# Performance work log

Measured on AMD Instinct MI355X. Metric: run time of the kernel, lower is better.

The kernel has to match this reference:

```python
import jax, jax.numpy as jnp
import numpy as np

N, G = 50000, 2500
PER = N // G                 # 20 nodes per graph
M, Z, NB, WIDTH, K = 128, 4, 8, 128, 3
INV = 3 * M                  # 384 invariant features
COV = 9 * M                  # 1152 = 128*(1+3+5)
GAMMA = 10.0
D_MIN, D_MAX = 0.9, 1.8
D_CENTER, D_HALF = 0.5 * (D_MIN + D_MAX), 0.5 * (D_MAX - D_MIN)
SQ_MZ = float(np.sqrt(M * Z))  # e3nn path normalization (fan_in = mul1*mul2)
P_GRID = 4096                # Fibonacci sphere quadrature for SO3 normalizer

_i = np.arange(P_GRID)
_ph = np.pi * (3.0 - np.sqrt(5.0)) * _i
_z = 1.0 - 2.0 * (_i + 0.5) / P_GRID
_r = np.sqrt(np.maximum(1.0 - _z * _z, 0.0))
FIB = np.stack([_r * np.cos(_ph), _r * np.sin(_ph), _z], 1).astype(np.float32)

def real_sh(v):
    # real spherical harmonics up to l=2, integral normalization, m=-l..l
    x, y, z = v[..., 0], v[..., 1], v[..., 2]
    c0, c1 = 0.28209479177387814, 0.4886025119029199
    ca, c20, c22 = 1.0925484305920792, 0.31539156525252005, 0.5462742152960396
    return jnp.stack([c0 * jnp.ones_like(x), c1 * y, c1 * z, c1 * x,
                      ca * x * y, ca * y * z, c20 * (3 * z * z - 1.0),
                      ca * x * z, c22 * (x * x - y * y)], -1)

Y_GRID = np.asarray(real_sh(jnp.asarray(FIB)))  # [P_GRID, 9]

def split_cov(x):
    lead = x.shape[:-1]
    return (x[..., :M].reshape(*lead, M, 1),
            x[..., M:4 * M].reshape(*lead, M, 3),
            x[..., 4 * M:9 * M].reshape(*lead, M, 5))

def setup_inputs():
    key = jax.random.key(0)
    ks = jax.random.split(key, 16)
    s_inter = jax.random.normal(ks[0], (N, COV), jnp.float32)
    bag = jnp.floor(jax.random.uniform(ks[1], (G, Z)) * 5.0).at[:, 0].add(1.0)
    batch = jnp.repeat(jnp.arange(G, dtype=jnp.int32), PER)
    ptr = jnp.arange(G + 1, dtype=jnp.int32) * PER
    focus = jax.random.randint(ks[2], (G,), 0, PER, jnp.int32)
    element = jnp.zeros((G,), jnp.int32)  # column 0 of bag is always > 0
    distance = D_MIN + (D_MAX - D_MIN) * jax.random.uniform(ks[3], (G,), jnp.float32)
    ori = jax.random.normal(ks[4], (G, 3), jnp.float32)
    orientation = ori / jnp.linalg.norm(ori, axis=-1, keepdims=True)
    W_bag = jax.random.normal(ks[5], (3, M, Z, M), jnp.float32)
    def lin(k, i, o):
        return jax.random.normal(k, (i, o), jnp.float32) / np.sqrt(i).astype(np.float32)
    return dict(
        s_inter=s_inter, bag=bag, batch=batch, ptr=ptr, focus=focus,
        element=element, distance=distance, orientation=orientation,
        W_bag=W_bag,
        d_log_stds=jnp.full((K,), np.log(0.1), jnp.float32),
        W_mix=jax.random.normal(ks[6], (NB, 3 * M * Z), jnp.float32),
        W1f=lin(ks[7], INV, WIDTH), b1f=jnp.zeros(WIDTH), W2f=lin(ks[8], WIDTH, 1), b2f=jnp.zeros(1),
        W1e=lin(ks[9], INV, WIDTH), b1e=jnp.zeros(WIDTH), W2e=lin(ks[10], WIDTH, Z), b2e=jnp.zeros(Z),
        W1d=lin(ks[11], INV + Z, WIDTH), b1d=jnp.zeros(WIDTH), W2d=lin(ks[12], WIDTH, 2 * K), b2d=jnp.zeros(2 * K),
    )

def reference(s_inter, bag, batch, ptr, focus, element, distance, orientation,
              W_bag, d_log_stds, W_mix,
              W1f, b1f, W2f, b2f, W1e, b1e, W2e, b2e, W1d, b1d, W2d, b2d):
    bag_n = bag[batch]                                  # [N, Z]
    xs = split_cov(s_inter)
    covs = [jnp.einsum('nim,nz,izo->nom', xs[l], bag_n, W_bag[l]) / SQ_MZ for l in range(3)]
    s_cov = jnp.concatenate([c.reshape(N, -1) for c in covs], -1)   # [N, 1152]
    s_inv = jnp.concatenate([jnp.sqrt(jnp.sum(c * c, -1) + 1e-12) for c in covs], -1)  # [N, 384]
    # --- focus: per-graph scatter softmax over nodes ---
    fl = (jax.nn.relu(s_inv @ W1f + b1f) @ W2f + b2f)[:, 0]
    mx = jax.ops.segment_max(fl, batch, num_segments=G)
    ex = jnp.exp(fl - mx[batch])
    focus_probs = ex / jax.ops.segment_sum(ex, batch, num_segments=G)[batch]
    gidx = focus + ptr[:-1]
    lp_focus = jnp.log(focus_probs[gidx] + 1e-20)
    # --- element: bag-masked softmax ---
    el = jax.nn.relu(s_inv @ W1e + b1e) @ W2e + b2e
    mask = (bag > 0)[batch]
    all_element_probs = jax.nn.softmax(jnp.where(mask, el, -1e9), -1)
    foc_el = all_element_probs[gidx]
    lp_element = jnp.log(jnp.take_along_axis(foc_el, element[:, None], 1)[:, 0] + 1e-20)
    element_oh = jax.nn.one_hot(element, Z, dtype=s_inter.dtype)
    # --- distance: Gaussian mixture head ---
    d_in = jnp.concatenate([s_inv[gidx], element_oh], -1)
    h = jax.nn.relu(d_in @ W1d + b1d) @ W2d + b2d
    gmm_logits, d_mean_t = h[:, :K], h[:, K:]
    d_mean = jnp.tanh(d_mean_t) * D_HALF + D_CENTER
    stds = jnp.maximum(jnp.exp(d_log_stds), 1e-6)
    logw = jax.nn.log_softmax(gmm_logits, -1)
    comp = -0.5 * ((distance[:, None] - d_mean) / stds) ** 2 - jnp.log(stds) - 0.5 * np.log(2 * np.pi).astype(np.float32)
    lp_dist = jax.nn.logsumexp(logw + comp, -1)
    # --- mix tensor product with bessel-conditioned external weights ---
    kk = jnp.arange(1, NB + 1, dtype=s_inter.dtype)
    bess = np.sqrt(2.0 / D_MAX).astype(np.float32) * jnp.sin(kk * np.pi * distance[:, None] / D_MAX) / distance[:, None]
    tpw = ((bess @ W_mix) / np.sqrt(NB).astype(np.float32)).reshape(G, 3, M, Z)
    foc = split_cov(s_cov[gidx])
    cond = [jnp.einsum('gim,gz,giz->gm', foc[l], element_oh, tpw[:, l]) / SQ_MZ for l in range(3)]
    cond_cov = jnp.concatenate(cond, -1)                # [G, 9]
    # --- SO(3) distribution: p(x) ~ exp(gamma * <a, Y(x)>), normalized on sphere grid ---
    ori = orientation / jnp.linalg.norm(orientation, axis=-1, keepdims=True)
    f_x = jnp.sum(cond_cov * real_sh(ori), -1)
    f_grid = cond_cov @ jnp.asarray(Y_GRID).T           # [G, P_GRID]
    logZ = jax.nn.logsumexp(GAMMA * f_grid, -1) - np.log(P_GRID).astype(np.float32) + np.log(4 * np.pi).astype(np.float32)
    lp_ori = GAMMA * f_x - logZ
    logp = lp_focus + lp_element + lp_dist + lp_ori
    # --- entropies: focus entropy + element|focus conditional entropy ---
    h_focus = -jax.ops.segment_sum(focus_probs * jnp.log(focus_probs + 1e-20), batch, num_segments=G)
    h_el = -jnp.sum(all_element_probs * jnp.log(jnp.maximum(all_element_probs, 1e-20)), -1)
    h_ef = jax.ops.segment_sum(focus_probs * h_el, batch, num_segments=G)
    entropy = h_focus + h_ef
    return jnp.stack([logp, entropy], -1)               # [G, 2]
```

## Files before the change

### kernel.cpp

```cpp
#include <hip/hip_runtime.h>
#include <math.h>

#define NN 50000
#define GG 2500
#define WS_YG    0
#define WS_SINV  36864
#define WS_FL    (WS_SINV + 19200000)
#define WS_HEL   (WS_FL + 50000)
#define WS_LPEL  (WS_HEL + 50000)
#define WS_SCOV  (WS_LPEL + 50000)
#define WS_TOTAL (WS_SCOV + 2880000)

__device__ __align__(16) float g_yg[4096 * 12];

__device__ __forceinline__ void real_sh9(float x, float y, float z, float* o) {
  const float c0 = 0.28209479177387814f;
  const float c1 = 0.4886025119029199f;
  const float ca = 1.0925484305920792f;
  const float c20 = 0.31539156525252005f;
  const float c22 = 0.5462742152960396f;
  o[0] = c0;
  o[1] = c1 * y;
  o[2] = c1 * z;
  o[3] = c1 * x;
  o[4] = ca * x * y;
  o[5] = ca * y * z;
  o[6] = c20 * (3.f * z * z - 1.f);
  o[7] = ca * x * z;
  o[8] = c22 * (x * x - y * y);
}

__global__ void k_ygrid() {
  int i = blockIdx.x * blockDim.x + threadIdx.x;
  if (i >= 4096) return;
  double fr = 0.38196601125010515 * (double)i;
  fr -= floor(fr);
  float ph = (float)(fr * 6.283185307179586);
  float z = 1.0f - 2.0f * ((float)i + 0.5f) * (1.0f / 4096.0f);
  float r = sqrtf(fmaxf(1.f - z * z, 0.f));
  float x = r * cosf(ph);
  float y = r * sinf(ph);
  float sh[9];
  real_sh9(x, y, z, sh);
#pragma unroll
  for (int m = 0; m < 9; ++m) g_yg[i * 12 + m] = sh[m];
  g_yg[i * 12 + 9] = 0.f;
  g_yg[i * 12 + 10] = 0.f;
  g_yg[i * 12 + 11] = 0.f;
}

#define FMA4(c, a, s)            \
  c.x = fmaf(a.x, s, c.x);       \
  c.y = fmaf(a.y, s, c.y);       \
  c.z = fmaf(a.z, s, c.z);       \
  c.w = fmaf(a.w, s, c.w);

#define EPI_M(ACC, M)                                                       \
  {                                                                         \
    const float e0 = ACC.x * invs, e1 = ACC.y * invs, e2 = ACC.z * invs,    \
                e3 = ACC.w * invs;                                          \
    sj0 += e0 * e0; sj1 += e1 * e1; sj2 += e2 * e2; sj3 += e3 * e3;         \
    if (isf) {                                                              \
      float* sp = scov + (size_t)g * 1152 + OFF + (size_t)o4 * COMP + (M);  \
      sp[0 * COMP] = e0; sp[1 * COMP] = e1;                                 \
      sp[2 * COMP] = e2; sp[3 * COMP] = e3;                                 \
    }                                                                       \
  }

template <int L, int COMP, int OFF>
__device__ __forceinline__ void cov_block(
    const float* __restrict__ X, const float* __restrict__ Wl,
    float b0, float b1, float b2, float b3,
    int n0, int nseg, int gi, int g,
    float* __restrict__ sinv, float* __restrict__ scov, float* A) {
  const int t = threadIdx.x;
  __syncthreads();
  for (int idx4 = t; idx4 < 4096; idx4 += 640) {
    const int i = idx4 >> 5, ol4 = (idx4 & 31) << 2;
    const float* wp = Wl + i * 512 + ol4;
    const float4 w0 = *(const float4*)(wp);
    const float4 w1 = *(const float4*)(wp + 128);
    const float4 w2 = *(const float4*)(wp + 256);
    const float4 w3 = *(const float4*)(wp + 384);
    float4 a;
    a.x = b0 * w0.x + b1 * w1.x + b2 * w2.x + b3 * w3.x;
    a.y = b0 * w0.y + b1 * w1.y + b2 * w2.y + b3 * w3.y;
    a.z = b0 * w0.z + b1 * w1.z + b2 * w2.z + b3 * w3.z;
    a.w = b0 * w0.w + b1 * w1.w + b2 * w2.w + b3 * w3.w;
    *(float4*)(A + i * 128 + ol4) = a;
  }
  __syncthreads();
  const int o4 = (t & 31) << 2;
  const int slot = t >> 5;
  if (slot < nseg) {
    const int n = n0 + slot;
    const float* xp = X + slot * 1152 + OFF;
    float4 ac0 = {0.f, 0.f, 0.f, 0.f};
    float4 ac1 = {0.f, 0.f, 0.f, 0.f};
    float4 ac2 = {0.f, 0.f, 0.f, 0.f};
    float4 ac3 = {0.f, 0.f, 0.f, 0.f};
    float4 ac4 = {0.f, 0.f, 0.f, 0.f};
    for (int i4 = 0; i4 < 128; i4 += 4) {
      const float* ap = A + i4 * 128 + o4;
      const float4 a0 = *(const float4*)(ap);
      const float4 a1 = *(const float4*)(ap + 128);
      const float4 a2 = *(const float4*)(ap + 256);
      const float4 a3 = *(const float4*)(ap + 384);
      if constexpr (COMP == 1) {
        const float4 x0 = *(const float4*)(xp + i4);
        FMA4(ac0, a0, x0.x);
        FMA4(ac0, a1, x0.y);
        FMA4(ac0, a2, x0.z);
        FMA4(ac0, a3, x0.w);
      } else if constexpr (COMP == 3) {
        const float* xq = xp + i4 * 3;
        const float4 x0 = *(const float4*)(xq);
        const float4 x1 = *(const float4*)(xq + 4);
        const float4 x2 = *(const float4*)(xq + 8);
        FMA4(ac0, a0, x0.x); FMA4(ac1, a0, x0.y); FMA4(ac2, a0, x0.z);
        FMA4(ac0, a1, x0.w); FMA4(ac1, a1, x1.x); FMA4(ac2, a1, x1.y);
        FMA4(ac0, a2, x1.z); FMA4(ac1, a2, x1.w); FMA4(ac2, a2, x2.x);
        FMA4(ac0, a3, x2.y); FMA4(ac1, a3, x2.z); FMA4(ac2, a3, x2.w);
      } else {
        const float* xq = xp + i4 * 5;
        const float4 x0 = *(const float4*)(xq);
        const float4 x1 = *(const float4*)(xq + 4);
        const float4 x2 = *(const float4*)(xq + 8);
        const float4 x3 = *(const float4*)(xq + 12);
        const float4 x4 = *(const float4*)(xq + 16);
        FMA4(ac0, a0, x0.x); FMA4(ac1, a0, x0.y); FMA4(ac2, a0, x0.z);
        FMA4(ac3, a0, x0.w); FMA4(ac4, a0, x1.x);
        FMA4(ac0, a1, x1.y); FMA4(ac1, a1, x1.z); FMA4(ac2, a1, x1.w);
        FMA4(ac3, a1, x2.x); FMA4(ac4, a1, x2.y);
        FMA4(ac0, a2, x2.z); FMA4(ac1, a2, x2.w); FMA4(ac2, a2, x3.x);
        FMA4(ac3, a2, x3.y); FMA4(ac4, a2, x3.z);
        FMA4(ac0, a3, x3.w); FMA4(ac1, a3, x4.x); FMA4(ac2, a3, x4.y);
        FMA4(ac3, a3, x4.z); FMA4(ac4, a3, x4.w);
      }
    }
    const bool isf = (n == gi);
    const float invs = 0.044194173824159216f;
    float sj0 = 1e-12f, sj1 = 1e-12f, sj2 = 1e-12f, sj3 = 1e-12f;
    EPI_M(ac0, 0);
    if constexpr (COMP > 1) {
      EPI_M(ac1, 1);
      EPI_M(ac2, 2);
    }
    if constexpr (COMP > 3) {
      EPI_M(ac3, 3);
      EPI_M(ac4, 4);
    }
    *(float4*)(sinv + (size_t)n * 384 + L * 128 + o4) =
        make_float4(sqrtf(sj0), sqrtf(sj1), sqrtf(sj2), sqrtf(sj3));
  }
}

__global__ __launch_bounds__(640) void k_cov(
    const float* __restrict__ s_inter, const float* __restrict__ bag,
    const int* __restrict__ ptr, const int* __restrict__ focus,
    const float* __restrict__ W_bag,
    float* __restrict__ sinv, float* __restrict__ scov) {
  __shared__ __align__(16) float A[16384];
  __shared__ __align__(16) float X[23040];
  const int g = blockIdx.x;
  const int t = threadIdx.x;
  const int n0 = ptr[g];
  const int nseg = ptr[g + 1] - n0;
  const int gi = n0 + focus[g];
  const float b0 = bag[g * 4 + 0], b1 = bag[g * 4 + 1];
  const float b2 = bag[g * 4 + 2], b3 = bag[g * 4 + 3];
  for (int idx = t; idx < 5760; idx += 640) {
    const int p = idx / 288;
    const int q4 = (idx - p * 288) << 2;
    if (p < nseg)
      *(float4*)(X + p * 1152 + q4) =
          *(const float4*)(s_inter + (size_t)(n0 + p) * 1152 + q4);
  }
  cov_block<0, 1, 0>(X, W_bag, b0, b1, b2, b3, n0, nseg, gi, g, sinv, scov, A);
  cov_block<1, 3, 128>(X, W_bag + 65536, b0, b1, b2, b3, n0, nseg, gi, g, sinv, scov, A);
  cov_block<2, 5, 512>(X, W_bag + 131072, b0, b1, b2, b3, n0, nseg, gi, g, sinv, scov, A);
}

__global__ __launch_bounds__(128) void k_mlp(
    const float* __restrict__ sinv, const float* __restrict__ bag,
    const int* __restrict__ batch, const int* __restrict__ element,
    const float* __restrict__ W1f, const float* __restrict__ b1f,
    const float* __restrict__ W2f, const float* __restrict__ b2f,
    const float* __restrict__ W1e, const float* __restrict__ b1e,
    const float* __restrict__ W2e, const float* __restrict__ b2e,
    float* __restrict__ flv, float* __restrict__ helv, float* __restrict__ lpelv) {
  __shared__ __align__(16) float lds[4224];
  __shared__ float els[32][4];
  const int t = threadIdx.x;
  const int n0 = blockIdx.x * 32;
  float af[32], ae[32];
#pragma unroll
  for (int p = 0; p < 32; ++p) { af[p] = 0.f; ae[p] = 0.f; }
  const float bf = b1f[t], be = b1e[t];
  for (int cb = 0; cb < 6; ++cb) {
    const int c0 = cb * 64;
    __syncthreads();
#pragma unroll
    for (int k = 0; k < 4; ++k) {
      const int idx = t + k * 128;
      const int p = idx >> 4, q = (idx & 15) * 4;
      float4 v = make_float4(0.f, 0.f, 0.f, 0.f);
      if (n0 + p < NN)
        v = *(const float4*)(sinv + (size_t)(n0 + p) * 384 + c0 + q);
      *(float4*)(lds + p * 64 + q) = v;
    }
    __syncthreads();
    for (int cc = 0; cc < 64; cc += 4) {
      const int c = c0 + cc;
      const float wf0 = W1f[(c + 0) * 128 + t];
      const float wf1 = W1f[(c + 1) * 128 + t];
      const float wf2 = W1f[(c + 2) * 128 + t];
      const float wf3 = W1f[(c + 3) * 128 + t];
      const float we0 = W1e[(c + 0) * 128 + t];
      const float we1 = W1e[(c + 1) * 128 + t];
      const float we2 = W1e[(c + 2) * 128 + t];
      const float we3 = W1e[(c + 3) * 128 + t];
#pragma unroll
      for (int p = 0; p < 32; ++p) {
        const float4 s4 = *(const float4*)(lds + p * 64 + cc);
        af[p] = fmaf(s4.x, wf0, af[p]);
        af[p] = fmaf(s4.y, wf1, af[p]);
        af[p] = fmaf(s4.z, wf2, af[p]);
        af[p] = fmaf(s4.w, wf3, af[p]);
        ae[p] = fmaf(s4.x, we0, ae[p]);
        ae[p] = fmaf(s4.y, we1, ae[p]);
        ae[p] = fmaf(s4.z, we2, ae[p]);
        ae[p] = fmaf(s4.w, we3, ae[p]);
      }
    }
  }
  __syncthreads();
#pragma unroll
  for (int p = 0; p < 32; ++p) lds[p * 132 + t] = fmaxf(af[p] + bf, 0.f);
  __syncthreads();
  if (t < 32) {
    float s = 0.f;
    for (int j = 0; j < 128; ++j) s = fmaf(lds[t * 132 + j], W2f[j], s);
    if (n0 + t < NN) flv[n0 + t] = s + b2f[0];
  }
  __syncthreads();
#pragma unroll
  for (int p = 0; p < 32; ++p) lds[p * 132 + t] = fmaxf(ae[p] + be, 0.f);
  __syncthreads();
  {
    const int p = t >> 2, z = t & 3;
    float s = 0.f;
    for (int j = 0; j < 128; ++j) s = fmaf(lds[p * 132 + j], W2e[j * 4 + z], s);
    els[p][z] = s + b2e[z];
  }
  __syncthreads();
  if (t < 32) {
    const int n = n0 + t;
    if (n < NN) {
      const int g = batch[n];
      const int elem = element[g];
      float v[4];
#pragma unroll
      for (int z = 0; z < 4; ++z) {
        const bool mk = bag[g * 4 + z] > 0.f;
        v[z] = mk ? els[t][z] : -1e9f;
      }
      const float mx = fmaxf(fmaxf(v[0], v[1]), fmaxf(v[2], v[3]));
      float e[4];
      float S = 0.f;
#pragma unroll
      for (int z = 0; z < 4; ++z) { e[z] = expf(v[z] - mx); S += e[z]; }
      const float iS = 1.f / S;
      float h = 0.f;
#pragma unroll
      for (int z = 0; z < 4; ++z) {
        const float pz = e[z] * iS;
        h -= pz * logf(fmaxf(pz, 1e-20f));
      }
      helv[n] = h;
      lpelv[n] = logf(e[elem] * iS + 1e-20f);
    }
  }
}

__global__ __launch_bounds__(128) void k_group(
    const int* __restrict__ ptr, const int* __restrict__ focus,
    const int* __restrict__ element, const float* __restrict__ distance,
    const float* __restrict__ orientation, const float* __restrict__ dls,
    const float* __restrict__ W_mix,
    const float* __restrict__ W1d, const float* __restrict__ b1d,
    const float* __restrict__ W2d, const float* __restrict__ b2d,
    const float* __restrict__ flv, const float* __restrict__ helv,
    const float* __restrict__ lpelv, const float* __restrict__ sinv,
    const float* __restrict__ scov,
    float* __restrict__ out) {
  __shared__ float fls[32];
  __shared__ float hels[32];
  __shared__ __align__(16) float svg[384];
  __shared__ float hd[128];
  __shared__ float out6[6];
  __shared__ float red[128][12];
  __shared__ float conds[9];
  __shared__ float mred[128];
  __shared__ float sred[128];
  const int g = blockIdx.x;
  const int t = threadIdx.x;
  const int n0 = ptr[g];
  const int nseg = ptr[g + 1] - n0;
  const int floc = focus[g];
  const int gi = n0 + floc;
  const int elem = element[g];
  const float dist = distance[g];
  if (t < nseg) { fls[t] = flv[n0 + t]; hels[t] = helv[n0 + t]; }
  for (int c = t; c < 384; c += 128) svg[c] = sinv[(size_t)gi * 384 + c];
  __syncthreads();
  float res_lpf = 0.f, res_ent = 0.f;
  if (t == 0) {
    float mx = -1e30f;
    for (int p = 0; p < nseg; ++p) mx = fmaxf(mx, fls[p]);
    float S = 0.f;
    for (int p = 0; p < nseg; ++p) S += expf(fls[p] - mx);
    const float iS = 1.f / S;
    float hfoc = 0.f, hef = 0.f;
    for (int p = 0; p < nseg; ++p) {
      const float pp = expf(fls[p] - mx) * iS;
      hfoc -= pp * logf(pp + 1e-20f);
      hef += pp * hels[p];
    }
    res_lpf = logf(expf(fls[floc] - mx) * iS + 1e-20f);
    res_ent = hfoc + hef;
  }
  {
    float acc = b1d[t];
    for (int c = 0; c < 384; c += 4) {
      const float4 s4 = *(const float4*)(&svg[c]);
      acc = fmaf(s4.x, W1d[(c + 0) * 128 + t], acc);
      acc = fmaf(s4.y, W1d[(c + 1) * 128 + t], acc);
      acc = fmaf(s4.z, W1d[(c + 2) * 128 + t], acc);
      acc = fmaf(s4.w, W1d[(c + 3) * 128 + t], acc);
    }
    acc += W1d[(384 + elem) * 128 + t];
    hd[t] = fmaxf(acc, 0.f);
  }
  __syncthreads();
  if (t < 6) {
    float s = 0.f;
    for (int j = 0; j < 128; ++j) s = fmaf(hd[j], W2d[j * 6 + t], s);
    out6[t] = s + b2d[t];
  }
  {
    float bess[8];
    const float sq2d = 1.0540925533894598f;
#pragma unroll
    for (int k = 0; k < 8; ++k)
      bess[k] = sq2d * sinf((float)(k + 1) * 3.14159265358979323846f * dist / 1.8f) / dist;
    const float invnb = 0.35355339059327373f;
    float partial[9];
    {
      float tw = 0.f;
#pragma unroll
      for (int k = 0; k < 8; ++k) tw += bess[k] * W_mix[k * 1536 + t * 4 + elem];
      tw *= invnb;
      partial[0] = scov[(size_t)g * 1152 + t] * tw;
    }
    {
      float tw = 0.f;
#pragma unroll
      for (int k = 0; k < 8; ++k) tw += bess[k] * W_mix[k * 1536 + (128 + t) * 4 + elem];
      tw *= invnb;
#pragma unroll
      for (int m = 0; m < 3; ++m) partial[1 + m] = scov[(size_t)g * 1152 + 128 + t * 3 + m] * tw;
    }
    {
      float tw = 0.f;
#pragma unroll
      for (int k = 0; k < 8; ++k) tw += bess[k] * W_mix[k * 1536 + (256 + t) * 4 + elem];
      tw *= invnb;
#pragma unroll
      for (int m = 0; m < 5; ++m) partial[4 + m] = scov[(size_t)g * 1152 + 512 + t * 5 + m] * tw;
    }
#pragma unroll
    for (int q = 0; q < 9; ++q) red[t][q] = partial[q];
  }
  __syncthreads();
  if (t < 9) {
    float s = 0.f;
    for (int i = 0; i < 128; ++i) s += red[i][t];
    conds[t] = s * 0.044194173824159216f;
  }
  __syncthreads();
  const float c0 = conds[0], c1 = conds[1], c2 = conds[2], c3 = conds[3];
  const float c4 = conds[4], c5 = conds[5], c6 = conds[6], c7 = conds[7];
  const float c8 = conds[8];
  float lm = -1e30f, ls = 0.f;
  for (int p = t; p < 4096; p += 128) {
    const float* yp = g_yg + p * 12;
    const float4 y0 = *(const float4*)(yp);
    const float4 y1 = *(const float4*)(yp + 4);
    const float4 y2 = *(const float4*)(yp + 8);
    float v = c0 * y0.x + c1 * y0.y + c2 * y0.z + c3 * y0.w + c4 * y1.x +
              c5 * y1.y + c6 * y1.z + c7 * y1.w + c8 * y2.x;
    v *= 10.0f;
    if (v > lm) { ls = ls * expf(lm - v) + 1.f; lm = v; }
    else ls += expf(v - lm);
  }
  mred[t] = lm;
  sred[t] = ls;
  __syncthreads();
  if (t == 0) {
    const float l0 = out6[0], l1 = out6[1], l2 = out6[2];
    const float lmx = fmaxf(l0, fmaxf(l1, l2));
    const float lsew = lmx + logf(expf(l0 - lmx) + expf(l1 - lmx) + expf(l2 - lmx));
    float vals[3];
#pragma unroll
    for (int k = 0; k < 3; ++k) {
      const float mean = tanhf(out6[3 + k]) * 0.45f + 1.35f;
      const float sd = fmaxf(expf(dls[k]), 1e-6f);
      const float zz = (dist - mean) / sd;
      vals[k] = (out6[k] - lsew) + (-0.5f * zz * zz - logf(sd) - 0.9189385332046727f);
    }
    const float vm = fmaxf(vals[0], fmaxf(vals[1], vals[2]));
    const float lp_dist =
        vm + logf(expf(vals[0] - vm) + expf(vals[1] - vm) + expf(vals[2] - vm));
    float Mx = -1e30f;
    for (int i = 0; i < 128; ++i) Mx = fmaxf(Mx, mred[i]);
    float S = 0.f;
    for (int i = 0; i < 128; ++i) S += sred[i] * expf(mred[i] - Mx);
    const float logZ = Mx + logf(S) - 8.317766166719343f + 2.5310242469692907f;
    float ox = orientation[g * 3 + 0], oy = orientation[g * 3 + 1], oz = orientation[g * 3 + 2];
    const float inr = 1.f / sqrtf(ox * ox + oy * oy + oz * oz);
    ox *= inr; oy *= inr; oz *= inr;
    float sh[9];
    real_sh9(ox, oy, oz, sh);
    const float fx = c0 * sh[0] + c1 * sh[1] + c2 * sh[2] + c3 * sh[3] + c4 * sh[4] +
                     c5 * sh[5] + c6 * sh[6] + c7 * sh[7] + c8 * sh[8];
    const float lp_ori = 10.0f * fx - logZ;
    out[g * 2 + 0] = res_lpf + lpelv[gi] + lp_dist + lp_ori;
    out[g * 2 + 1] = res_ent;
  }
}

extern "C" void kernel_launch(void* const* d_in, const int* in_sizes, int n_in,
                              void* d_out, int out_size, void* d_ws, size_t ws_size,
                              hipStream_t stream) {
  const float* s_inter = (const float*)d_in[0];
  const float* bag = (const float*)d_in[1];
  const int* batch = (const int*)d_in[2];
  const int* ptr = (const int*)d_in[3];
  const int* focus = (const int*)d_in[4];
  const int* element = (const int*)d_in[5];
  const float* distance = (const float*)d_in[6];
  const float* orientation = (const float*)d_in[7];
  const float* W_bag = (const float*)d_in[8];
  const float* dls = (const float*)d_in[9];
  const float* W_mix = (const float*)d_in[10];
  const float* W1f = (const float*)d_in[11];
  const float* b1f = (const float*)d_in[12];
  const float* W2f = (const float*)d_in[13];
  const float* b2f = (const float*)d_in[14];
  const float* W1e = (const float*)d_in[15];
  const float* b1e = (const float*)d_in[16];
  const float* W2e = (const float*)d_in[17];
  const float* b2e = (const float*)d_in[18];
  const float* W1d = (const float*)d_in[19];
  const float* b1d = (const float*)d_in[20];
  const float* W2d = (const float*)d_in[21];
  const float* b2d = (const float*)d_in[22];

  if (ws_size < (size_t)WS_TOTAL * sizeof(float)) return;

  float* ws = (float*)d_ws;
  float* sinv = ws + WS_SINV;
  float* flv = ws + WS_FL;
  float* helv = ws + WS_HEL;
  float* lpelv = ws + WS_LPEL;
  float* scov = ws + WS_SCOV;
  float* out = (float*)d_out;

  k_ygrid<<<dim3(32), dim3(128), 0, stream>>>();
  k_cov<<<dim3(GG), dim3(640), 0, stream>>>(s_inter, bag, ptr, focus, W_bag, sinv, scov);
  k_mlp<<<dim3((NN + 31) / 32), dim3(128), 0, stream>>>(sinv, bag, batch, element,
                                                        W1f, b1f, W2f, b2f,
                                                        W1e, b1e, W2e, b2e,
                                                        flv, helv, lpelv);
  k_group<<<dim3(GG), dim3(128), 0, stream>>>(ptr, focus, element, distance, orientation,
                                              dls, W_mix, W1d, b1d, W2d, b2d,
                                              flv, helv, lpelv, sinv, scov, out);
}
```

Measured before the change: 917.7 us.

## Register-tile the MLP first layer as 8 rows by 4 hidden units per thread

Each thread of the first MLP layer now computes an 8-node by 4-hidden-unit tile instead of all 32 nodes for a single hidden unit. Weights are read as float4 and each LDS float4 of activations is reused across 4 outputs, so far fewer LDS reads are issued per FMA. The accumulator count per thread stays at 64, so register pressure should be similar. The ReLU stores to LDS become float4 writes. The change relies on an FMA4 macro that is assumed to be defined in the unseen part of the file.

```diff
diff --git a/kernel.cpp b/kernel.cpp
--- a/kernel.cpp
+++ b/kernel.cpp
@@ -181,6 +181,31 @@
   cov_block<2, 5, 512>(X, W_bag + 131072, b0, b1, b2, b3, n0, nseg, gi, g, sinv, scov, A);
 }
 
+
+#define MLP_C(K, CM)                                                      \
+  {                                                                       \
+    const float4 wf = *(const float4*)(W1f + (c + K) * 128 + h4);         \
+    const float4 we = *(const float4*)(W1e + (c + K) * 128 + h4);         \
+    FMA4(af0, wf, s0.CM); FMA4(ae0, we, s0.CM);                           \
+    FMA4(af1, wf, s1.CM); FMA4(ae1, we, s1.CM);                           \
+    FMA4(af2, wf, s2.CM); FMA4(ae2, we, s2.CM);                           \
+    FMA4(af3, wf, s3.CM); FMA4(ae3, we, s3.CM);                           \
+    FMA4(af4, wf, s4.CM); FMA4(ae4, we, s4.CM);                           \
+    FMA4(af5, wf, s5.CM); FMA4(ae5, we, s5.CM);                           \
+    FMA4(af6, wf, s6.CM); FMA4(ae6, we, s6.CM);                           \
+    FMA4(af7, wf, s7.CM); FMA4(ae7, we, s7.CM);                           \
+  }
+
+#define STORE_H(A, J, B4)                                                 \
+  {                                                                       \
+    float4 r;                                                             \
+    r.x = fmaxf(A.x + B4.x, 0.f);                                         \
+    r.y = fmaxf(A.y + B4.y, 0.f);                                         \
+    r.z = fmaxf(A.z + B4.z, 0.f);                                         \
+    r.w = fmaxf(A.w + B4.w, 0.f);                                         \
+    *(float4*)(lds + (nrow0 + (J)) * 132 + h4) = r;                       \
+  }
+
 __global__ __launch_bounds__(128) void k_mlp(
     const float* __restrict__ sinv, const float* __restrict__ bag,
     const int* __restrict__ batch, const int* __restrict__ element,
@@ -193,10 +218,14 @@
   __shared__ float els[32][4];
   const int t = threadIdx.x;
   const int n0 = blockIdx.x * 32;
-  float af[32], ae[32];
-#pragma unroll
-  for (int p = 0; p < 32; ++p) { af[p] = 0.f; ae[p] = 0.f; }
-  const float bf = b1f[t], be = b1e[t];
+  const int hc = t & 31;
+  const int hr = t >> 5;
+  const int h4 = hc << 2;
+  const int nrow0 = hr << 3;
+  float4 af0 = {0,0,0,0}, af1 = {0,0,0,0}, af2 = {0,0,0,0}, af3 = {0,0,0,0};
+  float4 af4 = {0,0,0,0}, af5 = {0,0,0,0}, af6 = {0,0,0,0}, af7 = {0,0,0,0};
+  float4 ae0 = {0,0,0,0}, ae1 = {0,0,0,0}, ae2 = {0,0,0,0}, ae3 = {0,0,0,0};
+  float4 ae4 = {0,0,0,0}, ae5 = {0,0,0,0}, ae6 = {0,0,0,0}, ae7 = {0,0,0,0};
   for (int cb = 0; cb < 6; ++cb) {
     const int c0 = cb * 64;
     __syncthreads();
@@ -212,31 +241,27 @@
     __syncthreads();
     for (int cc = 0; cc < 64; cc += 4) {
       const int c = c0 + cc;
-      const float wf0 = W1f[(c + 0) * 128 + t];
-      const float wf1 = W1f[(c + 1) * 128 + t];
-      const float wf2 = W1f[(c + 2) * 128 + t];
-      const float wf3 = W1f[(c + 3) * 128 + t];
-      const float we0 = W1e[(c + 0) * 128 + t];
-      const float we1 = W1e[(c + 1) * 128 + t];
-      const float we2 = W1e[(c + 2) * 128 + t];
-      const float we3 = W1e[(c + 3) * 128 + t];
-#pragma unroll
-      for (int p = 0; p < 32; ++p) {
-        const float4 s4 = *(const float4*)(lds + p * 64 + cc);
-        af[p] = fmaf(s4.x, wf0, af[p]);
-        af[p] = fmaf(s4.y, wf1, af[p]);
-        af[p] = fmaf(s4.z, wf2, af[p]);
-        af[p] = fmaf(s4.w, wf3, af[p]);
-        ae[p] = fmaf(s4.x, we0, ae[p]);
-        ae[p] = fmaf(s4.y, we1, ae[p]);
-        ae[p] = fmaf(s4.z, we2, ae[p]);
-        ae[p] = fmaf(s4.w, we3, ae[p]);
-      }
-    }
-  }
-  __syncthreads();
-#pragma unroll
-  for (int p = 0; p < 32; ++p) lds[p * 132 + t] = fmaxf(af[p] + bf, 0.f);
+      const float* sb = lds + nrow0 * 64 + cc;
+      const float4 s0 = *(const float4*)(sb);
+      const float4 s1 = *(const float4*)(sb + 64);
+      const float4 s2 = *(const float4*)(sb + 128);
+      const float4 s3 = *(const float4*)(sb + 192);
+      const float4 s4 = *(const float4*)(sb + 256);
+      const float4 s5 = *(const float4*)(sb + 320);
+      const float4 s6 = *(const float4*)(sb + 384);
+      const float4 s7 = *(const float4*)(sb + 448);
+      MLP_C(0, x)
+      MLP_C(1, y)
+      MLP_C(2, z)
+      MLP_C(3, w)
+    }
+  }
+  const float4 bf4 = *(const float4*)(b1f + h4);
+  const float4 be4 = *(const float4*)(b1e + h4);
+  __syncthreads();
+  STORE_H(af0, 0, bf4) STORE_H(af1, 1, bf4) STORE_H(af2, 2, bf4)
+  STORE_H(af3, 3, bf4) STORE_H(af4, 4, bf4) STORE_H(af5, 5, bf4)
+  STORE_H(af6, 6, bf4) STORE_H(af7, 7, bf4)
   __syncthreads();
   if (t < 32) {
     float s = 0.f;
@@ -244,8 +269,9 @@
     if (n0 + t < NN) flv[n0 + t] = s + b2f[0];
   }
   __syncthreads();
-#pragma unroll
-  for (int p = 0; p < 32; ++p) lds[p * 132 + t] = fmaxf(ae[p] + be, 0.f);
+  STORE_H(ae0, 0, be4) STORE_H(ae1, 1, be4) STORE_H(ae2, 2, be4)
+  STORE_H(ae3, 3, be4) STORE_H(ae4, 4, be4) STORE_H(ae5, 5, be4)
+  STORE_H(ae6, 6, be4) STORE_H(ae7, 7, be4)
   __syncthreads();
   {
     const int p = t >> 2, z = t & 3;
```

Result: no change. 932.8 us (+1.6%).
